# Performance work log

Measured on AMD Instinct MI355X. Metric: run time of the kernel, lower is better.

The kernel has to match this reference:

```python
import jax, jax.numpy as jnp
import numpy as np

EPS = 1e-5
_BN_SCALE = 1.0 / float(np.sqrt(1.0 + EPS))  # eval-mode BN with running_mean=0, running_var=1


def _bn(x, g, b, axis):
    shp = [1] * x.ndim
    shp[axis] = -1
    return x * (g * _BN_SCALE).reshape(shp) + b.reshape(shp)


def setup_inputs() -> dict:
    key = jax.random.key(0)
    ks = jax.random.split(key, 24)
    D, NE, NR, H, NEdge, B = 200, 50000, 2000, 100000, 600000, 2048
    N = NE + 6
    NF, KH, KW = 200, 7, 3
    feat = NF * (D - KW + 1)  # 200*198 = 39600
    s = 0.02
    inp = {}
    inp['E'] = jax.random.normal(ks[0], (N, D), jnp.float32) * s
    inp['R'] = jax.random.normal(ks[1], (NR, D), jnp.float32) * s
    inp['w_alle'] = jax.random.normal(ks[2], (6 * D, D), jnp.float32) * s
    inp['w_addpos'] = jax.random.normal(ks[3], (2 * D, D), jnp.float32) * s
    inp['w_alleandr'] = jax.random.normal(ks[4], (D, D), jnp.float32) * s
    inp['w_rel'] = jax.random.normal(ks[5], (D, D), jnp.float32) * s
    inp['conv_w'] = jax.random.normal(ks[6], (NF, 1, KH, KW), jnp.float32) * s
    inp['conv_b'] = jnp.zeros((NF,), jnp.float32)
    inp['fc_w'] = jax.random.normal(ks[7], (feat, D), jnp.float32) * s
    inp['fc_b'] = jnp.zeros((D,), jnp.float32)
    inp['bnmp_g'] = jnp.ones((D,), jnp.float32)
    inp['bnmp_b'] = jnp.zeros((D,), jnp.float32)
    inp['bn0_g'] = jnp.ones((1,), jnp.float32)
    inp['bn0_b'] = jnp.zeros((1,), jnp.float32)
    inp['bn1_g'] = jnp.ones((NF,), jnp.float32)
    inp['bn1_b'] = jnp.zeros((NF,), jnp.float32)
    inp['bn2_g'] = jnp.ones((D,), jnp.float32)
    inp['bn2_b'] = jnp.zeros((D,), jnp.float32)
    inp['ms'] = jnp.ones((B, 6), jnp.float32)
    he_r = jax.random.randint(ks[8], (H, 1), 0, NR)
    he_e = jax.random.randint(ks[9], (H, 6), 0, N)
    inp['hyperedge'] = jnp.concatenate([he_r, he_e], axis=1)
    inp['edge_index'] = jax.random.randint(ks[10], (2, NEdge), 0, N)
    inp['edge_type'] = jax.random.randint(ks[11], (NEdge,), 0, H)
    inp['r_idx'] = jax.random.randint(ks[12], (B,), 0, NR)
    for k, nm in enumerate(['e1_idx', 'e2_idx', 'e3_idx', 'e4_idx', 'e5_idx', 'e6_idx']):
        inp[nm] = jax.random.randint(ks[13 + k], (B,), 0, NE)
    inp['ent_num'] = NE
    return inp


def reference(E, R, w_alle, w_addpos, w_alleandr, w_rel, conv_w, conv_b, fc_w, fc_b,
              bnmp_g, bnmp_b, bn0_g, bn0_b, bn1_g, bn1_b, bn2_g, bn2_b, ms,
              hyperedge, edge_index, edge_type, r_idx,
              e1_idx, e2_idx, e3_idx, e4_idx, e5_idx, e6_idx, ent_num):
    N, D = E.shape
    pos = E[ent_num:ent_num + 6]                      # [6, D] positional embeddings
    # --- MP layer: hyperedge embeddings ---
    r_he = R[hyperedge[:, 0]]                         # [H, D]
    eh = E[hyperedge[:, 1:7]] * pos[None]             # [H, 6, D]
    e_all = eh.reshape(eh.shape[0], 6 * D) @ w_alle   # [H, D]
    hemb = (0.5 * e_all + 0.5 * r_he) @ w_alleandr    # [H, D]
    # --- message: gather-concat-matmul, scatter-add aggregation ---
    msg = jnp.concatenate([hemb[edge_type], E[edge_index[1]]], axis=1) @ w_addpos  # [Ne, D]
    agg = jax.ops.segment_sum(msg, edge_index[0], num_segments=N)                  # [N, D]
    outE = jnp.tanh(_bn(0.5 * agg + 0.5 * E, bnmp_g, bnmp_b, 1))
    outR = R @ w_rel
    # --- ConvE-style scoring head ---
    qpos = outE[ent_num:ent_num + 6]
    es = [outE[idx] * qpos[k][None] * ms[:, k:k + 1]
          for k, idx in enumerate([e1_idx, e2_idx, e3_idx, e4_idx, e5_idx, e6_idx])]
    stk = jnp.stack([outR[r_idx]] + es, axis=1)[:, None]  # [B, 1, 7, D]
    x = _bn(stk, bn0_g, bn0_b, 1)
    x = jax.lax.conv_general_dilated(x, conv_w, (1, 1), 'VALID',
                                     dimension_numbers=('NCHW', 'OIHW', 'NCHW'))
    x = x + conv_b[None, :, None, None]               # [B, 200, 1, 198]
    x = jax.nn.relu(_bn(x, bn1_g, bn1_b, 1))
    x = x.reshape(x.shape[0], -1)                     # [B, 39600]
    x = x @ fc_w + fc_b
    x = jax.nn.relu(_bn(x, bn2_g, bn2_b, 1))
    return jnp.sum(x, axis=1)                         # [B]
```

## Files before the change

### kernel.cpp

```cpp
#include <hip/hip_runtime.h>

#define D 200
#define FEAT 39600
#define BNS_F 0.9999950000374997f
#define FC_NSPLIT 16
#define BHALF 1024

typedef float f32x4 __attribute__((ext_vector_type(4)));
typedef short s16x8 __attribute__((ext_vector_type(8)));
typedef unsigned int u32;

static __device__ __forceinline__ unsigned short f2b(float f) {
  union { float f; unsigned u; } v; v.f = f;
  return (unsigned short)((v.u + 0x7FFFu + ((v.u >> 16) & 1u)) >> 16);
}
static __device__ __forceinline__ float b2f(unsigned short h) {
  union { unsigned u; float f; } v; v.u = ((unsigned)h) << 16;
  return v.f;
}
static __device__ __forceinline__ void gload_lds16(const void* g, void* l) {
  __builtin_amdgcn_global_load_lds((const __attribute__((address_space(1))) u32*)g,
                                   (__attribute__((address_space(3))) u32*)l, 16, 0, 0);
}


__global__ __launch_bounds__(256) void k_cvt_bf16(const float* __restrict__ src,
                                                  unsigned short* __restrict__ dst, int n) {
  int stride = gridDim.x * 256;
  for (int i = blockIdx.x * 256 + threadIdx.x; i < n; i += stride) dst[i] = f2b(src[i]);
}

__global__ __launch_bounds__(256) void k_sgemm(const float* __restrict__ A, const float* __restrict__ Bm,
                                               float* __restrict__ C, int M,
                                               const float* __restrict__ rowscale, float scale) {
  __shared__ float A8[8][200];
  int tid = threadIdx.x;
  int m0 = blockIdx.x * 8;
  for (int u = tid; u < 8 * 200; u += 256) {
    int m = u / 200, k = u - m * 200;
    A8[m][k] = (m0 + m < M) ? A[(size_t)(m0 + m) * 200 + k] : 0.f;
  }
  __syncthreads();
  int j = tid; if (j >= 200) return;
  float acc[8] = {0,0,0,0,0,0,0,0};
  for (int u = 0; u < 200; ++u) {
    float b = Bm[u * 200 + j];
#pragma unroll
    for (int m = 0; m < 8; ++m) acc[m] += A8[m][u] * b;
  }
#pragma unroll
  for (int m = 0; m < 8; ++m) {
    int r = m0 + m;
    if (r < M) {
      float s = scale * (rowscale ? rowscale[r] : 1.f);
      C[(size_t)r * 200 + j] = acc[m] * s;
    }
  }
}

__global__ __launch_bounds__(64) void k_packB(const float* __restrict__ T, const float* __restrict__ w_addpos,
                                              unsigned short* __restrict__ out, int NT, int kofs, int useG) {
  int blk = blockIdx.x;
  int lane = threadIdx.x;
  int nt = blk % NT, kt = blk / NT;
  int col = nt * 16 + (lane & 15);
  unsigned short* p = out + (size_t)blk * 512 + lane * 8;
#pragma unroll
  for (int t = 0; t < 8; ++t) {
    int kk = kt * 32 + ((lane >> 4) << 3) + t;
    float v = 0.f;
    if (kk < 200) {
      if (col < 600) {
        int k = col / 200;
        v = T[(size_t)((kofs + k) * 200 + kk) * 200 + (col - k * 200)];
      } else if (useG && col < 800) {
        v = w_addpos[(size_t)(200 + kk) * 200 + (col - 600)];
      }
    }
    p[t] = f2b(v);
  }
}

__global__ __launch_bounds__(64) void k_prep_wfc(const float* __restrict__ fc_w,
                                                 unsigned short* __restrict__ Wpk, int K) {
  int blk = blockIdx.x;
  int lane = threadIdx.x;
  int nt = blk % 13; int kt = blk / 13;
  int j = nt * 16 + (lane & 15);
  unsigned short* p = Wpk + (size_t)blk * 512 + lane * 8;
#pragma unroll
  for (int t = 0; t < 8; ++t) {
    int kk = kt * 32 + ((lane >> 4) << 3) + t;
    float v = (kk < K && j < D) ? fc_w[(size_t)kk * D + j] : 0.f;
    p[t] = f2b(v);
  }
}


__global__ __launch_bounds__(256) void k_mask(const int* __restrict__ e1, const int* __restrict__ e2,
                                              const int* __restrict__ e3, const int* __restrict__ e4,
                                              const int* __restrict__ e5, const int* __restrict__ e6,
                                              int ent, int* __restrict__ needed, int B) {
  int t = blockIdx.x * 256 + threadIdx.x;
  int total = 6 * B;
  if (t < total) {
    int k = t / B, b = t - k * B;
    const int* p = (k == 0) ? e1 : (k == 1) ? e2 : (k == 2) ? e3 : (k == 3) ? e4 : (k == 4) ? e5 : e6;
    needed[p[b]] = 1;
  } else if (t < total + 6) {
    needed[ent + (t - total)] = 1;
  }
}

__global__ __launch_bounds__(256) void k_compact(int* __restrict__ needed,
                                                 int* __restrict__ list, int* __restrict__ cnt, int Nn) {
  int n = blockIdx.x * 256 + threadIdx.x;
  if (n < Nn && needed[n]) {
    int p = atomicAdd(cnt, 1);
    list[p] = n;
    needed[n] = p + 1;
  }
}

__global__ __launch_bounds__(256) void k_ecount(const int* __restrict__ esrc, const int* __restrict__ needed,
                                                int* __restrict__ deg, int* __restrict__ epos, int NEdge) {
  int e = blockIdx.x * 256 + threadIdx.x;
  if (e >= NEdge) return;
  int sl = needed[esrc[e]];
  epos[e] = (sl > 0) ? atomicAdd(&deg[sl - 1], 1) : -1;
}

__global__ __launch_bounds__(256) void k_prefix(const int* __restrict__ deg, int* __restrict__ rowstart, int nslot) {
  __shared__ int csum[256];
  int t = threadIdx.x;
  int chunk = (nslot + 255) / 256;
  int b = t * chunk;
  int s = 0;
  for (int i = 0; i < chunk; ++i) { int idx = b + i; if (idx < nslot) s += deg[idx]; }
  csum[t] = s;
  __syncthreads();
  if (t == 0) {
    int run = 0;
    for (int i = 0; i < 256; ++i) { int x = csum[i]; csum[i] = run; run += x; }
  }
  __syncthreads();
  int run = csum[t];
  for (int i = 0; i < chunk; ++i) {
    int idx = b + i;
    if (idx < nslot) { rowstart[idx] = run; run += deg[idx]; }
  }
}

__global__ __launch_bounds__(256) void k_efill(const int* __restrict__ esrc, const int* __restrict__ needed,
                                               const int* __restrict__ rowstart, const int* __restrict__ epos,
                                               int* __restrict__ elist, int NEdge) {
  int e = blockIdx.x * 256 + threadIdx.x;
  if (e >= NEdge) return;
  int p = epos[e];
  if (p >= 0) {
    int sl = needed[esrc[e]] - 1;
    elist[rowstart[sl] + p] = e;
  }
}


#define P_LDA 116

__global__ __launch_bounds__(256) void k_pgemm(const u32* __restrict__ Ebf32,
                                               const unsigned short* __restrict__ Wbp,
                                               unsigned short* __restrict__ Pv, int NT) {
  __shared__ u32 Alds[64 * P_LDA];
  int tid = threadIdx.x, lane = tid & 63, wid = tid >> 6;
  size_t m0 = (size_t)blockIdx.x * 64;
  for (int u = tid; u < 64 * P_LDA; u += 256) {
    int r = u / P_LDA, c = u - r * P_LDA;
    u32 val = 0;
    if (c < 100) val = Ebf32[(m0 + r) * 100 + c];
    Alds[u] = val;
  }
  __syncthreads();
  const unsigned short* Abf = (const unsigned short*)Alds;
  int np = NT >> 1;
  for (int p = wid; p < np; p += 4) {
    f32x4 acc[2][4];
#pragma unroll
    for (int h = 0; h < 2; ++h)
#pragma unroll
      for (int rt = 0; rt < 4; ++rt) acc[h][rt] = (f32x4){0.f, 0.f, 0.f, 0.f};
#pragma unroll
    for (int kt = 0; kt < 7; ++kt) {
      s16x8 afr[4];
#pragma unroll
      for (int rt = 0; rt < 4; ++rt)
        afr[rt] = *(const s16x8*)(Abf + (rt * 16 + (lane & 15)) * (P_LDA * 2) + kt * 32 + ((lane >> 4) << 3));
#pragma unroll
      for (int h = 0; h < 2; ++h) {
        int nt = p * 2 + h;
        s16x8 bfr = *(const s16x8*)(Wbp + ((size_t)(kt * NT + nt)) * 512 + lane * 8);
#pragma unroll
        for (int rt = 0; rt < 4; ++rt)
          acc[h][rt] = __builtin_amdgcn_mfma_f32_16x16x32_bf16(afr[rt], bfr, acc[h][rt], 0, 0, 0);
      }
    }
#pragma unroll
    for (int h = 0; h < 2; ++h) {
      int colb = (p * 2 + h) * 16 + (lane & 15);
#pragma unroll
      for (int rt = 0; rt < 4; ++rt) {
#pragma unroll
        for (int r = 0; r < 4; ++r) {
          int row = rt * 16 + ((lane >> 4) << 2) + r;
          Pv[(m0 + row) * 800 + colb] = f2b(acc[rt == rt ? h : h][rt][r]);
        }
      }
    }
  }
}


__global__ __launch_bounds__(128) void k_vsum(const u32* __restrict__ Pv32, const float* __restrict__ Rv,
                                              const int* __restrict__ he, u32* __restrict__ V32, int kbase) {
  int h = blockIdx.x;
  int c = threadIdx.x;
  if (c >= 100) return;
  const int* hrow = he + (size_t)h * 7;
  float ax, ay;
  if (kbase == 0) {
    int r = hrow[0];
    ax = Rv[(size_t)r * 200 + 2 * c];
    ay = Rv[(size_t)r * 200 + 2 * c + 1];
  } else {
    u32 v = V32[(size_t)h * 100 + c];
    ax = b2f((unsigned short)v);
    ay = b2f((unsigned short)(v >> 16));
  }
#pragma unroll
  for (int k = 0; k < 3; ++k) {
    int e = hrow[1 + kbase + k];
    u32 g = Pv32[(size_t)e * 400 + k * 100 + c];
    ax += b2f((unsigned short)g);
    ay += b2f((unsigned short)(g >> 16));
  }
  V32[(size_t)h * 100 + c] = ((u32)f2b(ay) << 16) | (u32)f2b(ax);
}


__global__ __launch_bounds__(128) void k_gagg(const int* __restrict__ list, const int* __restrict__ cnt,
                                              const int* __restrict__ deg, const int* __restrict__ rowstart,
                                              const int* __restrict__ elist, const int* __restrict__ etyp,
                                              const int* __restrict__ edst,
                                              const u32* __restrict__ V32, const u32* __restrict__ Pv32,
                                              const float* __restrict__ E,
                                              const float* __restrict__ bnmp_g, const float* __restrict__ bnmp_b,
                                              float* __restrict__ outEc) {
  int slot = blockIdx.x;
  if (slot >= *cnt) return;
  int c = threadIdx.x;
  if (c >= 100) return;
  int n = list[slot];
  int nE = deg[slot];
  int rs = rowstart[slot];
  float ax = 0.f, ay = 0.f;
  for (int i = 0; i < nE; ++i) {
    int e = elist[rs + i];
    int et = etyp[e], dd = edst[e];
    u32 v = V32[(size_t)et * 100 + c];
    u32 g = Pv32[(size_t)dd * 400 + 300 + c];
    ax += b2f((unsigned short)v) + b2f((unsigned short)g);
    ay += b2f((unsigned short)(v >> 16)) + b2f((unsigned short)(g >> 16));
  }
  int j = 2 * c;
  float gx = bnmp_g[j] * BNS_F, bx = bnmp_b[j];
  float gy = bnmp_g[j + 1] * BNS_F, by = bnmp_b[j + 1];
  float ex = E[(size_t)n * 200 + j], ey = E[(size_t)n * 200 + j + 1];
  float ox = tanhf((0.5f * ax + 0.5f * ex) * gx + bx);
  float oy = tanhf((0.5f * ay + 0.5f * ey) * gy + by);
  *(float2*)(outEc + (size_t)slot * 200 + j) = make_float2(ox, oy);
}


__global__ __launch_bounds__(256) void k_stk(const float* __restrict__ outEc, const float* __restrict__ outR,
                                             const int* __restrict__ needed,
                                             const int* __restrict__ r_idx,
                                             const int* __restrict__ e1, const int* __restrict__ e2,
                                             const int* __restrict__ e3, const int* __restrict__ e4,
                                             const int* __restrict__ e5, const int* __restrict__ e6,
                                             const float* __restrict__ ms, int ent,
                                             const float* __restrict__ bn0_g, const float* __restrict__ bn0_b,
                                             float* __restrict__ stk) {
  int b = blockIdx.x; int j = threadIdx.x;
  if (j >= D) return;
  float s0 = bn0_g[0] * BNS_F, b0 = bn0_b[0];
  float* out = stk + (size_t)b * 1400;
  out[j] = outR[(size_t)r_idx[b] * D + j] * s0 + b0;
#pragma unroll
  for (int k = 0; k < 6; ++k) {
    const int* ep = (k == 0) ? e1 : (k == 1) ? e2 : (k == 2) ? e3 : (k == 3) ? e4 : (k == 4) ? e5 : e6;
    int slotq = needed[ent + k] - 1;
    int slote = needed[ep[b]] - 1;
    float q = outEc[(size_t)slotq * D + j];
    float v = outEc[(size_t)slote * D + j] * q * ms[(size_t)b * 6 + k];
    out[(1 + k) * D + j] = v * s0 + b0;
  }
}


__global__ __launch_bounds__(256) void k_conv(const float* __restrict__ stk, const float* __restrict__ conv_w,
                                              const float* __restrict__ conv_b, const float* __restrict__ bn1_g,
                                              const float* __restrict__ bn1_b, unsigned short* __restrict__ x1,
                                              int KPAD, int b0) {
  __shared__ float srow[1400];
  __shared__ float cw[4200];
  __shared__ float cb[200], g1[200], b1[200];
  int b = blockIdx.x, tid = threadIdx.x;
  for (int u = tid; u < 1400; u += 256) srow[u] = stk[(size_t)(b0 + b) * 1400 + u];
  for (int u = tid; u < 4200; u += 256) cw[u] = conv_w[u];
  if (tid < 200) { cb[tid] = conv_b[tid]; g1[tid] = bn1_g[tid] * BNS_F; b1[tid] = bn1_b[tid]; }
  __syncthreads();
  for (int idx = tid; idx < FEAT; idx += 256) {
    int f = idx / 198, w = idx - f * 198;
    float acc = 0.f;
#pragma unroll
    for (int kh = 0; kh < 7; ++kh)
#pragma unroll
      for (int kw = 0; kw < 3; ++kw)
        acc += srow[kh * 200 + w + kw] * cw[f * 21 + kh * 3 + kw];
    float v = (acc + cb[f]) * g1[f] + b1[f];
    v = v > 0.f ? v : 0.f;
    x1[(size_t)b * KPAD + idx] = f2b(v);
  }
  for (int idx = FEAT + tid; idx < KPAD; idx += 256) x1[(size_t)b * KPAD + idx] = 0;
}


__global__ __launch_bounds__(256) void k_fcgemm(const u32* __restrict__ X32,
                                                const unsigned short* __restrict__ Wpk,
                                                float* __restrict__ Ypart,
                                                int Mtot, int KU32, int KCH, int chPerSeg) {
  __shared__ u32 Alds[2][2048];
  int tid = threadIdx.x;
  int lane = tid & 63, wid = tid >> 6;
  int mblks = gridDim.x / FC_NSPLIT;
  int seg = blockIdx.x / mblks;
  int mblk = blockIdx.x - seg * mblks;
  int row0 = mblk * 32;
  int ch0 = seg * chPerSeg;
  int nCh = KCH - ch0; if (nCh > chPerSeg) nCh = chPerSeg;
  if (nCh <= 0) return;

  int nt0 = (wid == 0) ? 0 : (wid == 1) ? 4 : (wid == 2) ? 7 : 10;
  int ntc = (wid == 0) ? 4 : 3;

  f32x4 acc[2][4];
#pragma unroll
  for (int a = 0; a < 2; ++a)
#pragma unroll
    for (int b = 0; b < 4; ++b) acc[a][b] = (f32x4){0.f, 0.f, 0.f, 0.f};

  int srow0 = tid >> 4;
  int slch0 = (tid & 15) ^ (srow0 & 7);
  int srow1 = (tid + 256) >> 4;
  int slch1 = (tid & 15) ^ (srow1 & 7);
  int gr0 = row0 + srow0; if (gr0 >= Mtot) gr0 = Mtot - 1;
  int gr1 = row0 + srow1; if (gr1 >= Mtot) gr1 = Mtot - 1;
  const u32* src0 = X32 + (size_t)gr0 * KU32 + slch0 * 4;
  const u32* src1 = X32 + (size_t)gr1 * KU32 + slch1 * 4;

#define STAGE(bsel, ch)                                                        \
  do {                                                                         \
    gload_lds16(src0 + (size_t)(ch) * 64, &Alds[bsel][wid * 256]);             \
    gload_lds16(src1 + (size_t)(ch) * 64, &Alds[bsel][1024 + wid * 256]);      \
  } while (0)

  STAGE(0, ch0);
  __syncthreads();

  for (int i = 0; i < nCh; ++i) {
    if (i + 1 < nCh) STAGE((i + 1) & 1, ch0 + i + 1);
    const unsigned short* buf = (const unsigned short*)Alds[i & 1];
    int ch = ch0 + i;
#pragma unroll
    for (int kkt = 0; kkt < 4; ++kkt) {
      s16x8 afr[2];
#pragma unroll
      for (int rt = 0; rt < 2; ++rt) {
        int row = rt * 16 + (lane & 15);
        int pch = ((kkt << 2) + (lane >> 4)) ^ (row & 7);
        afr[rt] = *(const s16x8*)(buf + row * 128 + pch * 8);
      }
      size_t ktg = (size_t)(ch * 4 + kkt);
#pragma unroll
      for (int ln = 0; ln < 4; ++ln) {
        if (ln < ntc) {
          s16x8 bfr = *(const s16x8*)(Wpk + (ktg * 13 + nt0 + ln) * 512 + lane * 8);
          acc[0][ln] = __builtin_amdgcn_mfma_f32_16x16x32_bf16(afr[0], bfr, acc[0][ln], 0, 0, 0);
          acc[1][ln] = __builtin_amdgcn_mfma_f32_16x16x32_bf16(afr[1], bfr, acc[1][ln], 0, 0, 0);
        }
      }
    }
    __syncthreads();
  }
#undef STAGE

  float* Yp = Ypart + (size_t)seg * Mtot * 208;
#pragma unroll
  for (int rt = 0; rt < 2; ++rt) {
#pragma unroll
    for (int ln = 0; ln < 4; ++ln) {
      if (ln < ntc) {
        int j = (nt0 + ln) * 16 + (lane & 15);
#pragma unroll
        for (int r = 0; r < 4; ++r) {
          int b = row0 + rt * 16 + ((lane >> 4) << 2) + r;
          if (b < Mtot) Yp[(size_t)b * 208 + j] = acc[rt][ln][r];
        }
      }
    }
  }
}


__global__ __launch_bounds__(256) void k_epilogue(const float* __restrict__ Ypart, const float* __restrict__ fc_b,
                                                  const float* __restrict__ bn2_g, const float* __restrict__ bn2_b,
                                                  float* __restrict__ out, int Mtot, int b0) {
  __shared__ float red[4];
  int b = blockIdx.x, tid = threadIdx.x;
  float v = 0.f;
  if (tid < D) {
    float y = fc_b[tid];
#pragma unroll
    for (int s = 0; s < FC_NSPLIT; ++s) y += Ypart[((size_t)s * Mtot + b) * 208 + tid];
    y = y * (bn2_g[tid] * BNS_F) + bn2_b[tid];
    v = y > 0.f ? y : 0.f;
  }
#pragma unroll
  for (int o = 32; o > 0; o >>= 1) v += __shfl_down(v, o);
  if ((tid & 63) == 0) red[tid >> 6] = v;
  __syncthreads();
  if (tid == 0) out[b0 + b] = red[0] + red[1] + red[2] + red[3];
}


extern "C" void kernel_launch(void* const* d_in, const int* in_sizes, int n_in,
                              void* d_out, int out_size, void* d_ws, size_t ws_size,
                              hipStream_t stream) {
  const float* E          = (const float*)d_in[0];
  const float* R          = (const float*)d_in[1];
  const float* w_alle     = (const float*)d_in[2];
  const float* w_addpos   = (const float*)d_in[3];
  const float* w_alleandr = (const float*)d_in[4];
  const float* w_rel      = (const float*)d_in[5];
  const float* conv_w     = (const float*)d_in[6];
  const float* conv_b     = (const float*)d_in[7];
  const float* fc_w       = (const float*)d_in[8];
  const float* fc_b       = (const float*)d_in[9];
  const float* bnmp_g     = (const float*)d_in[10];
  const float* bnmp_b     = (const float*)d_in[11];
  const float* bn0_g      = (const float*)d_in[12];
  const float* bn0_b      = (const float*)d_in[13];
  const float* bn1_g      = (const float*)d_in[14];
  const float* bn1_b      = (const float*)d_in[15];
  const float* bn2_g      = (const float*)d_in[16];
  const float* bn2_b      = (const float*)d_in[17];
  const float* ms         = (const float*)d_in[18];
  const int* hyperedge    = (const int*)d_in[19];
  const int* edge_index   = (const int*)d_in[20];
  const int* edge_type    = (const int*)d_in[21];
  const int* r_idx        = (const int*)d_in[22];
  const int* e1 = (const int*)d_in[23];
  const int* e2 = (const int*)d_in[24];
  const int* e3 = (const int*)d_in[25];
  const int* e4 = (const int*)d_in[26];
  const int* e5 = (const int*)d_in[27];
  const int* e6 = (const int*)d_in[28];

  const int Nn    = in_sizes[0] / D;
  const int NR    = in_sizes[1] / D;
  const int Hh    = in_sizes[19] / 7;
  const int NEdge = in_sizes[21];
  const int B     = in_sizes[22];
  const int ent   = Nn - 6;
  const int K_fc  = in_sizes[8] / D;
  const int KCH   = (K_fc + 127) / 128;
  const int KPAD  = KCH * 128;
  const int KU32  = KPAD / 2;
  const int chPerSeg = (KCH + FC_NSPLIT - 1) / FC_NSPLIT;
  const int KT_tot = KCH * 4;
  const int NSLOT = 6 * B + 6;
  const int MPAD  = ((Nn + 63) / 64) * 64;
  const int NT_A = 38, NT_B = 50;

  const int* esrc = edge_index;
  const int* edst = edge_index + NEdge;

  char* W = (char*)d_ws;
  size_t off = 0;
  auto alloc = [&](size_t bytes) { size_t o = off; off += (bytes + 255) & ~(size_t)255; return o; };
  size_t o_Wfc  = alloc((size_t)KT_tot * 13 * 512 * 2);
  size_t o_WbpA = alloc((size_t)7 * NT_A * 512 * 2);
  size_t o_WbpB = alloc((size_t)7 * NT_B * 512 * 2);
  size_t o_Wtop = alloc((size_t)200 * 200 * 4);
  size_t o_T    = alloc((size_t)1200 * 200 * 4);
  size_t o_Rv   = alloc((size_t)NR * 200 * 4);
  size_t o_outR = alloc((size_t)NR * 200 * 4);
  size_t o_need = alloc(((size_t)Nn + 1) * 4);
  size_t o_list = alloc((size_t)NSLOT * 4 + 64);
  size_t o_deg  = alloc((size_t)NSLOT * 4 + 64);
  size_t o_rs   = alloc((size_t)NSLOT * 4 + 64);
  size_t o_epos = alloc((size_t)NEdge * 4);
  size_t o_elist= alloc((size_t)NEdge * 4);
  size_t o_outEc= alloc((size_t)NSLOT * 200 * 4);
  size_t o_stk  = alloc((size_t)B * 1400 * 4);
  size_t o_A    = off;
  size_t o_Pv   = alloc((size_t)MPAD * 800 * 2);
  size_t o_V    = alloc((size_t)Hh * 200 * 2);
  size_t o_Ebf  = alloc((size_t)MPAD * 200 * 2);
  size_t regionA_end = off;

  size_t x1_bytes = (size_t)BHALF * KPAD * 2;
  size_t o_x1 = o_A;
  size_t o_Yp = o_A + ((x1_bytes + 255) & ~(size_t)255);
  size_t yp_bytes = (size_t)FC_NSPLIT * BHALF * 208 * 4;
  if (ws_size < off) return;
  if (o_Yp + yp_bytes > regionA_end) return;

  unsigned short* Wfc  = (unsigned short*)(W + o_Wfc);
  unsigned short* WbpA = (unsigned short*)(W + o_WbpA);
  unsigned short* WbpB = (unsigned short*)(W + o_WbpB);
  float* Wtop  = (float*)(W + o_Wtop);
  float* T     = (float*)(W + o_T);
  float* Rv    = (float*)(W + o_Rv);
  float* outR  = (float*)(W + o_outR);
  int*   needed= (int*)(W + o_need);
  int*   cnt   = needed + Nn;
  int*   list  = (int*)(W + o_list);
  int*   deg   = (int*)(W + o_deg);
  int*   rs    = (int*)(W + o_rs);
  int*   epos  = (int*)(W + o_epos);
  int*   elist = (int*)(W + o_elist);
  float* outEc = (float*)(W + o_outEc);
  float* stk   = (float*)(W + o_stk);
  unsigned short* Pv  = (unsigned short*)(W + o_Pv);
  unsigned short* Vb  = (unsigned short*)(W + o_V);
  unsigned short* Ebf = (unsigned short*)(W + o_Ebf);
  unsigned short* x1  = (unsigned short*)(W + o_x1);
  float* Ypart        = (float*)(W + o_Yp);

  hipMemsetAsync(needed, 0, ((size_t)Nn + 1) * 4, stream);
  hipMemsetAsync(deg, 0, (size_t)NSLOT * 4, stream);

  hipLaunchKernelGGL(k_cvt_bf16, dim3(4096), dim3(256), 0, stream, E, Ebf, Nn * D);
  hipLaunchKernelGGL(k_sgemm, dim3(25), dim3(256), 0, stream, w_alleandr, w_addpos, Wtop, 200, (const float*)nullptr, 1.0f);
  hipLaunchKernelGGL(k_sgemm, dim3(150), dim3(256), 0, stream, w_alle, Wtop, T, 1200, E + (size_t)ent * D, 0.5f);
  hipLaunchKernelGGL(k_sgemm, dim3(250), dim3(256), 0, stream, R, Wtop, Rv, NR, (const float*)nullptr, 0.5f);
  hipLaunchKernelGGL(k_sgemm, dim3(250), dim3(256), 0, stream, R, w_rel, outR, NR, (const float*)nullptr, 1.0f);
  hipLaunchKernelGGL(k_packB, dim3(7 * NT_A), dim3(64), 0, stream, T, w_addpos, WbpA, NT_A, 0, 0);
  hipLaunchKernelGGL(k_packB, dim3(7 * NT_B), dim3(64), 0, stream, T, w_addpos, WbpB, NT_B, 3, 1);
  hipLaunchKernelGGL(k_prep_wfc, dim3(KT_tot * 13), dim3(64), 0, stream, fc_w, Wfc, K_fc);

  hipLaunchKernelGGL(k_mask, dim3((6 * B + 6 + 255) / 256), dim3(256), 0, stream,
                     e1, e2, e3, e4, e5, e6, ent, needed, B);
  hipLaunchKernelGGL(k_compact, dim3((Nn + 255) / 256), dim3(256), 0, stream, needed, list, cnt, Nn);
  hipLaunchKernelGGL(k_ecount, dim3((NEdge + 255) / 256), dim3(256), 0, stream, esrc, needed, deg, epos, NEdge);
  hipLaunchKernelGGL(k_prefix, dim3(1), dim3(256), 0, stream, deg, rs, NSLOT);
  hipLaunchKernelGGL(k_efill, dim3((NEdge + 255) / 256), dim3(256), 0, stream, esrc, needed, rs, epos, elist, NEdge);

  hipLaunchKernelGGL(k_pgemm, dim3(MPAD / 64), dim3(256), 0, stream, (const u32*)Ebf, WbpA, Pv, NT_A);
  hipLaunchKernelGGL(k_vsum, dim3(Hh), dim3(128), 0, stream, (const u32*)Pv, Rv, hyperedge, (u32*)Vb, 0);
  hipLaunchKernelGGL(k_pgemm, dim3(MPAD / 64), dim3(256), 0, stream, (const u32*)Ebf, WbpB, Pv, NT_B);
  hipLaunchKernelGGL(k_vsum, dim3(Hh), dim3(128), 0, stream, (const u32*)Pv, Rv, hyperedge, (u32*)Vb, 3);

  hipLaunchKernelGGL(k_gagg, dim3(NSLOT), dim3(128), 0, stream,
                     list, cnt, deg, rs, elist, edge_type, edst,
                     (const u32*)Vb, (const u32*)Pv, E, bnmp_g, bnmp_b, outEc);

  hipLaunchKernelGGL(k_stk, dim3(B), dim3(256), 0, stream,
                     outEc, outR, needed, r_idx, e1, e2, e3, e4, e5, e6, ms, ent, bn0_g, bn0_b, stk);

  for (int half = 0; half < 2; ++half) {
    int b0 = half * BHALF;
    hipLaunchKernelGGL(k_conv, dim3(BHALF), dim3(256), 0, stream, stk, conv_w, conv_b, bn1_g, bn1_b, x1, KPAD, b0);
    hipLaunchKernelGGL(k_fcgemm, dim3((BHALF / 32) * FC_NSPLIT), dim3(256), 0, stream,
                       (const u32*)x1, Wfc, Ypart, BHALF, KU32, KCH, chPerSeg);
    hipLaunchKernelGGL(k_epilogue, dim3(BHALF), dim3(256), 0, stream, Ypart, fc_b, bn2_g, bn2_b, (float*)d_out, BHALF, b0);
  }
}
```

Measured before the change: 977.9 us.

## Register-block conv over width strips and permute FC weights to w-major layout

Result: faster. 896.9 us (-8.3%).

```diff
diff --git a/kernel.cpp b/kernel.cpp
--- a/kernel.cpp
+++ b/kernel.cpp
@@ -91,7 +91,8 @@
 #pragma unroll
   for (int t = 0; t < 8; ++t) {
     int kk = kt * 32 + ((lane >> 4) << 3) + t;
-    float v = (kk < K && j < D) ? fc_w[(size_t)kk * D + j] : 0.f;
+    int w = kk / 200, f = kk - w * 200;
+    float v = (w < 198 && j < D) ? fc_w[(size_t)(f * 198 + w) * D + j] : 0.f;
     p[t] = f2b(v);
   }
 }
@@ -210,7 +211,7 @@
 #pragma unroll
         for (int r = 0; r < 4; ++r) {
           int row = rt * 16 + ((lane >> 4) << 2) + r;
-          Pv[(m0 + row) * 800 + colb] = f2b(acc[rt == rt ? h : h][rt][r]);
+          Pv[(m0 + row) * 800 + colb] = f2b(acc[h][rt][r]);
         }
       }
     }
@@ -309,27 +310,55 @@
                                               const float* __restrict__ conv_b, const float* __restrict__ bn1_g,
                                               const float* __restrict__ bn1_b, unsigned short* __restrict__ x1,
                                               int KPAD, int b0) {
-  __shared__ float srow[1400];
+  __shared__ float srow[1408];
   __shared__ float cw[4200];
   __shared__ float cb[200], g1[200], b1[200];
   int b = blockIdx.x, tid = threadIdx.x;
   for (int u = tid; u < 1400; u += 256) srow[u] = stk[(size_t)(b0 + b) * 1400 + u];
+  if (tid < 8) srow[1400 + tid] = 0.f;
   for (int u = tid; u < 4200; u += 256) cw[u] = conv_w[u];
   if (tid < 200) { cb[tid] = conv_b[tid]; g1[tid] = bn1_g[tid] * BNS_F; b1[tid] = bn1_b[tid]; }
   __syncthreads();
-  for (int idx = tid; idx < FEAT; idx += 256) {
-    int f = idx / 198, w = idx - f * 198;
-    float acc = 0.f;
+  int lane = tid & 63, wid = tid >> 6;
+  unsigned short* xrow = x1 + (size_t)b * KPAD;
+  for (int strip = wid; strip < 25; strip += 4) {
+    int w0 = strip * 8;
+    int nw = 198 - w0; if (nw > 8) nw = 8;
+    float sreg[7][10];
 #pragma unroll
     for (int kh = 0; kh < 7; ++kh)
 #pragma unroll
-      for (int kw = 0; kw < 3; ++kw)
-        acc += srow[kh * 200 + w + kw] * cw[f * 21 + kh * 3 + kw];
-    float v = (acc + cb[f]) * g1[f] + b1[f];
-    v = v > 0.f ? v : 0.f;
-    x1[(size_t)b * KPAD + idx] = f2b(v);
-  }
-  for (int idx = FEAT + tid; idx < KPAD; idx += 256) x1[(size_t)b * KPAD + idx] = 0;
+      for (int i = 0; i < 10; ++i)
+        sreg[kh][i] = srow[kh * 200 + w0 + i];
+#pragma unroll
+    for (int q = 0; q < 4; ++q) {
+      int f = lane + q * 64;
+      if (f < 200) {
+        float acc[8];
+#pragma unroll
+        for (int i = 0; i < 8; ++i) acc[i] = 0.f;
+#pragma unroll
+        for (int kh = 0; kh < 7; ++kh) {
+          float c0 = cw[f * 21 + kh * 3 + 0];
+          float c1 = cw[f * 21 + kh * 3 + 1];
+          float c2 = cw[f * 21 + kh * 3 + 2];
+#pragma unroll
+          for (int i = 0; i < 8; ++i)
+            acc[i] += sreg[kh][i] * c0 + sreg[kh][i + 1] * c1 + sreg[kh][i + 2] * c2;
+        }
+        float gf = g1[f], bf = b1[f], cf = cb[f];
+#pragma unroll
+        for (int i = 0; i < 8; ++i) {
+          if (i < nw) {
+            float v = (acc[i] + cf) * gf + bf;
+            v = v > 0.f ? v : 0.f;
+            xrow[(size_t)(w0 + i) * 200 + f] = f2b(v);
+          }
+        }
+      }
+    }
+  }
+  for (int idx = FEAT + tid; idx < KPAD; idx += 256) xrow[idx] = 0;
 }
 
 
```
